# Kernel optimization log

Measured on AMD Instinct MI355X. Metric: run time of the kernel, lower is better.

Reference implementation:

```python
import jax, jax.numpy as jnp
import numpy as np

D_MODEL = 512
N_HEADS = 8
D_HEAD = D_MODEL // N_HEADS
N_LAYERS = 6
VOCAB = 32000
B, S = 4, 1024
EPS = 1e-5


def positional_encoding(length, d_model):
    # matches get_positional_encoding_table: pos * (1/10000**(i/d)), sin on even i, cos on odd i
    inv = 1.0 / (10000.0 ** (jnp.arange(d_model, dtype=jnp.float32) / d_model))
    ang = jnp.arange(length, dtype=jnp.float32)[:, None] * inv[None, :]  # [S, D]
    pe = jnp.where(jnp.arange(d_model) % 2 == 0, jnp.sin(ang), jnp.cos(ang))
    return pe


def layer_norm(x, g, b):
    m = jnp.mean(x, axis=-1, keepdims=True)
    v = jnp.mean((x - m) ** 2, axis=-1, keepdims=True)
    return (x - m) * jax.lax.rsqrt(v + EPS) * g + b


def setup_inputs() -> dict:
    key = jax.random.key(0)
    ks = jax.random.split(key, 9)
    sc = 0.02
    return {
        "tokens": jax.random.randint(ks[0], (B, S), 0, VOCAB),
        "emb": jax.random.normal(ks[1], (VOCAB, D_MODEL), jnp.float32) * sc,
        "Wq": jax.random.normal(ks[2], (N_LAYERS, D_MODEL, D_MODEL), jnp.float32) * sc,
        "bq": jnp.zeros((N_LAYERS, D_MODEL), jnp.float32),
        "Wk": jax.random.normal(ks[3], (N_LAYERS, D_MODEL, D_MODEL), jnp.float32) * sc,
        "bk": jnp.zeros((N_LAYERS, D_MODEL), jnp.float32),
        "Wv": jax.random.normal(ks[4], (N_LAYERS, D_MODEL, D_MODEL), jnp.float32) * sc,
        "bv": jnp.zeros((N_LAYERS, D_MODEL), jnp.float32),
        "Wo": jax.random.normal(ks[5], (N_LAYERS, D_MODEL, D_MODEL), jnp.float32) * sc,
        "bo": jnp.zeros((N_LAYERS, D_MODEL), jnp.float32),
        "W1": jax.random.normal(ks[6], (N_LAYERS, D_MODEL, 4 * D_MODEL), jnp.float32) * sc,
        "b1": jnp.zeros((N_LAYERS, 4 * D_MODEL), jnp.float32),
        "W2": jax.random.normal(ks[7], (N_LAYERS, 4 * D_MODEL, D_MODEL), jnp.float32) * sc,
        "b2": jnp.zeros((N_LAYERS, D_MODEL), jnp.float32),
        "ln_g": jnp.ones((N_LAYERS, D_MODEL), jnp.float32),
        "ln_b": jnp.zeros((N_LAYERS, D_MODEL), jnp.float32),
    }


def encoder_layer(x, Wq, bq, Wk, bk, Wv, bv, Wo, bo, W1, b1, W2, b2, g, b):
    bsz = x.shape[0]
    q = (x @ Wq + bq).reshape(bsz, -1, N_HEADS, D_HEAD).transpose(0, 2, 1, 3)  # [B,h,S,dk]
    k = (x @ Wk + bk).reshape(bsz, -1, N_HEADS, D_HEAD).transpose(0, 2, 1, 3)
    v = (x @ Wv + bv).reshape(bsz, -1, N_HEADS, D_HEAD).transpose(0, 2, 1, 3)
    scores = jnp.einsum('bhqd,bhkd->bhqk', q, k) / (D_HEAD ** 0.5)
    w = jax.nn.softmax(scores, axis=-1)
    attn = jnp.einsum('bhqk,bhkd->bhqd', w, v)  # [B,h,S,dv]
    # faithful to source bug: .view(B,-1,h*dv) WITHOUT transposing heads back
    attn = attn.reshape(bsz, -1, N_HEADS * D_HEAD)  # [B,S,D] with heads/seq interleaved
    x = layer_norm(x + (attn @ Wo + bo), g, b)
    ffn = jnp.maximum(x @ W1 + b1, 0.0) @ W2 + b2
    x = layer_norm(x + ffn, g, b)  # same (shared) LayerNorm params, as in source
    return x


def reference(tokens, emb, Wq, bq, Wk, bk, Wv, bv, Wo, bo, W1, b1, W2, b2, ln_g, ln_b):
    x = emb[tokens]  # [B,S,D]
    x = x + positional_encoding(x.shape[1], D_MODEL)
    for i in range(N_LAYERS):
        x = encoder_layer(x, Wq[i], bq[i], Wk[i], bk[i], Wv[i], bv[i], Wo[i], bo[i],
                          W1[i], b1[i], W2[i], b2[i], ln_g[i], ln_b[i])
    return x
```

## Files before the change

kernel.cpp:

```cpp
#include <hip/hip_runtime.h>
#include <hip/hip_bf16.h>
#include <math.h>

typedef unsigned short ushort_t;
typedef unsigned int uint_t;
typedef __attribute__((ext_vector_type(8))) short bfrag_t;
typedef __attribute__((ext_vector_type(4))) float facc_t;
typedef __attribute__((ext_vector_type(16))) float facc16_t;

#define D_MODEL 512
#define NH 8
#define DH 64
#define NL 6
#define BB 4
#define SS 1024
#define ROWS (BB*SS)
#define DFF 2048

__device__ inline ushort_t f2bf(float f) {
    __hip_bfloat16 h = __float2bfloat16(f);
    return *(ushort_t*)&h;
}
__device__ inline float bf2f(ushort_t u) {
    unsigned int x = ((unsigned int)u) << 16;
    union { unsigned int i; float f; } c; c.i = x;
    return c.f;
}
__device__ inline uint_t pkbf(float lo, float hi) {
    return (uint_t)f2bf(lo) | ((uint_t)f2bf(hi) << 16);
}
__device__ inline void gload_lds16(const void* g, void* l) {
    __builtin_amdgcn_global_load_lds((const __attribute__((address_space(1))) unsigned int*)g,
                                     (__attribute__((address_space(3))) unsigned int*)l, 16, 0, 0);
}

__global__ __launch_bounds__(256) void embed_pe(const int* __restrict__ tok,
                                                const float* __restrict__ emb,
                                                float* __restrict__ x,
                                                ushort_t* __restrict__ xbf) {
    int row = blockIdx.x;
    int s = row & (SS - 1);
    int t = tok[row];
    const float* e = emb + (size_t)t * D_MODEL;
    for (int i = threadIdx.x; i < D_MODEL; i += 256) {
        float freq = __expf(-9.210340371976184f * ((float)i / (float)D_MODEL));
        float ang = (float)s * freq;
        float pe = (i & 1) ? cosf(ang) : sinf(ang);
        float v = e[i] + pe;
        x[(size_t)row * D_MODEL + i] = v;
        xbf[(size_t)row * D_MODEL + i] = f2bf(v);
    }
}

__global__ __launch_bounds__(256) void prep_weights(const float* __restrict__ Wq,
                                                    const float* __restrict__ Wk,
                                                    const float* __restrict__ Wv,
                                                    const float* __restrict__ Wo,
                                                    const float* __restrict__ W1,
                                                    const float* __restrict__ W2,
                                                    int layer, ushort_t* __restrict__ wlay) {
    __shared__ float tile[32][33];
    int z = blockIdx.z;
    const float* src; ushort_t* dst; int K, N;
    size_t o512 = (size_t)layer * 512 * 512;
    size_t o1M  = (size_t)layer * 512 * 2048;
    switch (z) {
        case 0: src = Wq + o512; dst = wlay;               K = 512;  N = 512;  break;
        case 1: src = Wk + o512; dst = wlay + 262144;      K = 512;  N = 512;  break;
        case 2: src = Wv + o512; dst = wlay + 524288;      K = 512;  N = 512;  break;
        case 3: src = Wo + o512; dst = wlay + 786432;      K = 512;  N = 512;  break;
        case 4: src = W1 + o1M;  dst = wlay + 1048576;     K = 512;  N = 2048; break;
        default:src = W2 + o1M;  dst = wlay + 2097152;     K = 2048; N = 512;  break;
    }
    int n0 = blockIdx.x * 32, k0 = blockIdx.y * 32;
    if (n0 >= N || k0 >= K) return;
    int tx = threadIdx.x & 31, ty = threadIdx.x >> 5;
    #pragma unroll
    for (int i = 0; i < 4; i++)
        tile[ty + i * 8][tx] = src[(size_t)(k0 + ty + i * 8) * N + n0 + tx];
    __syncthreads();
    #pragma unroll
    for (int i = 0; i < 4; i++)
        dst[(size_t)(n0 + ty + i * 8) * K + k0 + tx] = f2bf(tile[tx][ty + i * 8]);
}

__global__ __launch_bounds__(256) void concat_bias(const float* __restrict__ bq,
                                                   const float* __restrict__ bk,
                                                   const float* __restrict__ bv,
                                                   float* __restrict__ bqkv) {
    int l = blockIdx.x;
    for (int i = threadIdx.x; i < 1536; i += 256) {
        float v = (i < 512) ? bq[l * 512 + i]
                : (i < 1024) ? bk[l * 512 + i - 512]
                : bv[l * 512 + i - 1024];
        bqkv[l * 1536 + i] = v;
    }
}

template<int BM, int BN>
__global__ __launch_bounds__(256) void gemm_pipe(const ushort_t* __restrict__ A,
                                                 const ushort_t* __restrict__ Bt,
                                                 const float* __restrict__ bias,
                                                 float* __restrict__ Cf,
                                                 ushort_t* __restrict__ Cb,
                                                 int N, int Ktot, int relu) {
    constexpr int TI = BM / 32, TJ = BN / 32;
    __shared__ ushort_t lA[2][BM * 64];
    __shared__ ushort_t lB[2][BN * 64];

    const int tid = threadIdx.x;
    const int w = tid >> 6, lane = tid & 63;
    const int wr = w & 1, wc = w >> 1;
    const int lane16 = lane & 15, quad = lane >> 4;
    const int row0 = blockIdx.y * BM, col0 = blockIdx.x * BN;

    facc_t acc[TI][TJ];
    #pragma unroll
    for (int i = 0; i < TI; i++)
        #pragma unroll
        for (int j = 0; j < TJ; j++)
            acc[i][j] = (facc_t){0.f, 0.f, 0.f, 0.f};

    auto stage = [&](int buf, int k0) {
        #pragma unroll
        for (int i = 0; i < BM / 32; i++) {
            int g = i * 256 + tid;
            int r = g >> 3, p = g & 7;
            int q = p ^ (r & 7);
            gload_lds16(A + (size_t)(row0 + r) * Ktot + k0 + q * 8,
                        lA[buf] + (size_t)g * 8);
        }
        #pragma unroll
        for (int i = 0; i < BN / 32; i++) {
            int g = i * 256 + tid;
            int r = g >> 3, p = g & 7;
            int q = p ^ (r & 7);
            gload_lds16(Bt + (size_t)(col0 + r) * Ktot + k0 + q * 8,
                        lB[buf] + (size_t)g * 8);
        }
    };
    auto compute = [&](int buf) {
        #pragma unroll
        for (int kk = 0; kk < 2; kk++) {
            bfrag_t af[TI], bf_[TJ];
            int q = kk * 4 + quad;
            #pragma unroll
            for (int t = 0; t < TI; t++) {
                int m = wr * (BM / 2) + t * 16 + lane16;
                af[t] = *(const bfrag_t*)(lA[buf] + ((size_t)m * 8 + (q ^ (m & 7))) * 8);
            }
            #pragma unroll
            for (int t = 0; t < TJ; t++) {
                int n = wc * (BN / 2) + t * 16 + lane16;
                bf_[t] = *(const bfrag_t*)(lB[buf] + ((size_t)n * 8 + (q ^ (n & 7))) * 8);
            }
            #pragma unroll
            for (int ti = 0; ti < TI; ti++)
                #pragma unroll
                for (int tj = 0; tj < TJ; tj++)
                    acc[ti][tj] = __builtin_amdgcn_mfma_f32_16x16x32_bf16(
                        af[ti], bf_[tj], acc[ti][tj], 0, 0, 0);
        }
    };

    const int nt = Ktot >> 6;
    stage(0, 0);
    __syncthreads();
    for (int t = 0; t < nt; t++) {
        if (t + 1 < nt) stage((t + 1) & 1, (t + 1) * 64);
        compute(t & 1);
        __syncthreads();
    }

    float bv_[TJ];
    #pragma unroll
    for (int tj = 0; tj < TJ; tj++)
        bv_[tj] = bias[col0 + wc * (BN / 2) + tj * 16 + lane16];

    #pragma unroll
    for (int ti = 0; ti < TI; ti++) {
        int grow = row0 + wr * (BM / 2) + ti * 16 + quad * 4;
        #pragma unroll
        for (int tj = 0; tj < TJ; tj++) {
            int gcol = col0 + wc * (BN / 2) + tj * 16 + lane16;
            #pragma unroll
            for (int rr = 0; rr < 4; rr++) {
                float v = acc[ti][tj][rr] + bv_[tj];
                if (relu) v = fmaxf(v, 0.f);
                size_t idx = (size_t)(grow + rr) * N + gcol;
                if (Cf) Cf[idx] = v;
                if (Cb) Cb[idx] = f2bf(v);
            }
        }
    }
}

__global__ __launch_bounds__(128) void attn_mfma_split(const ushort_t* __restrict__ qkv,
                                                       ushort_t* __restrict__ Yp,
                                                       float2* __restrict__ mlp) {
    __shared__ __align__(16) ushort_t lK[4096];
    __shared__ __align__(16) ushort_t lVT[2][4096];

    const int tid = threadIdx.x;
    const int w = tid >> 6, lane = tid & 63;
    const int l31 = lane & 31, H = lane >> 5;
    const int qt = blockIdx.x, h = blockIdx.y;
    const int b = blockIdx.z >> 1, kh = blockIdx.z & 1;
    const int kt0 = kh * 8;

    const float LOG2E = 1.4426950408889634f;
    const float SC = 0.125f * 1.4426950408889634f;

    const ushort_t* Qrow = qkv + (size_t)(b * SS + qt * 64 + w * 32 + l31) * 1536 + h * 64;
    bfrag_t qb[4];
    #pragma unroll
    for (int s = 0; s < 4; s++)
        qb[s] = *(const bfrag_t*)(Qrow + s * 16 + H * 8);

    facc16_t O0, O1;
    #pragma unroll
    for (int r = 0; r < 16; r++) { O0[r] = 0.f; O1[r] = 0.f; }
    float mrow = -INFINITY, lrow = 0.f;

    const int vkey = tid & 63;
    const int vdg  = tid >> 6;
    const int vk8 = vkey >> 3, vj = vkey & 7;

    auto stageK = [&](int kt) {
        #pragma unroll
        for (int i = 0; i < 4; i++) {
            int g = i * 128 + tid;
            int r = g >> 3, p = g & 7;
            int q = p ^ (r & 7);
            gload_lds16(qkv + (size_t)(b * SS + kt * 64 + r) * 1536 + h * 64 + 512 + q * 8,
                        lK + (size_t)g * 8);
        }
    };
    auto loadV = [&](int kt, ushort_t* vs) {
        const ushort_t* vsrc = qkv + (size_t)(b * SS + kt * 64 + vkey) * 1536
                               + h * 64 + 1024 + vdg * 32;
        #pragma unroll
        for (int i4 = 0; i4 < 4; i4++)
            *(uint4*)(vs + i4 * 8) = *(const uint4*)(vsrc + i4 * 8);
    };
    auto writeV = [&](const ushort_t* vs, int buf) {
        #pragma unroll
        for (int e = 0; e < 32; e++) {
            int n = vdg * 32 + e;
            lVT[buf][(size_t)(n * 8 + (vk8 ^ (n & 7))) * 8 + vj] = vs[e];
        }
    };

    {
        ushort_t v0[32];
        stageK(kt0);
        loadV(kt0, v0);
        writeV(v0, 0);
    }
    __syncthreads();

    for (int kt = kt0; kt < kt0 + 8; kt++) {
        const int buf = (kt - kt0) & 1;
        const bool more = (kt < kt0 + 7);

        ushort_t vn[32];
        if (more) loadV(kt + 1, vn);

        facc16_t sfv[2];
        #pragma unroll
        for (int half = 0; half < 2; half++) {
            facc16_t s_;
            #pragma unroll
            for (int r = 0; r < 16; r++) s_[r] = 0.f;
            int row = half * 32 + l31;
            #pragma unroll
            for (int s = 0; s < 4; s++) {
                int c = 2 * s + H;
                bfrag_t kf = *(const bfrag_t*)(lK + ((size_t)row * 8 + (c ^ (row & 7))) * 8);
                s_ = __builtin_amdgcn_mfma_f32_32x32x16_bf16(kf, qb[s], s_, 0, 0, 0);
            }
            sfv[half] = s_;
        }

        if (more) {
            __syncthreads();
            stageK(kt + 1);
        }

        #pragma unroll
        for (int half = 0; half < 2; half++) {
            facc16_t s_ = sfv[half];

            float mt = s_[0];
            #pragma unroll
            for (int r = 1; r < 16; r++) mt = fmaxf(mt, s_[r]);
            mt *= 0.125f;
            mt = fmaxf(mt, __shfl_xor(mt, 32));

            bool small = (mt <= mrow + 8.f);
            if (!__all(small)) {
                float mn = fmaxf(mrow, mt);
                float al = __builtin_amdgcn_exp2f((mrow - mn) * LOG2E);
                mrow = mn;
                lrow *= al;
                #pragma unroll
                for (int r = 0; r < 16; r++) { O0[r] *= al; O1[r] *= al; }
            }
            float mC = mrow * LOG2E;

            float p[16];
            float ps = 0.f;
            #pragma unroll
            for (int r = 0; r < 16; r++) {
                p[r] = __builtin_amdgcn_exp2f(fmaf(s_[r], SC, -mC));
                ps += p[r];
            }
            ps += __shfl_xor(ps, 32);
            lrow += ps;

            uint_t A0 = pkbf(p[0], p[1]),   A1 = pkbf(p[2], p[3]);
            uint_t B0 = pkbf(p[4], p[5]),   B1 = pkbf(p[6], p[7]);
            uint_t C0 = pkbf(p[8], p[9]),   C1 = pkbf(p[10], p[11]);
            uint_t D0 = pkbf(p[12], p[13]), D1 = pkbf(p[14], p[15]);
            uint_t XA0 = __shfl_xor(A0, 32), XA1 = __shfl_xor(A1, 32);
            uint_t XB0 = __shfl_xor(B0, 32), XB1 = __shfl_xor(B1, 32);
            uint_t XC0 = __shfl_xor(C0, 32), XC1 = __shfl_xor(C1, 32);
            uint_t XD0 = __shfl_xor(D0, 32), XD1 = __shfl_xor(D1, 32);

            union { bfrag_t v; uint_t u[4]; } pf0, pf1;
            pf0.u[0] = H ? XB0 : A0;  pf0.u[1] = H ? XB1 : A1;
            pf0.u[2] = H ? B0 : XA0;  pf0.u[3] = H ? B1 : XA1;
            pf1.u[0] = H ? XD0 : C0;  pf1.u[1] = H ? XD1 : C1;
            pf1.u[2] = H ? D0 : XC0;  pf1.u[3] = H ? D1 : XC1;

            #pragma unroll
            for (int t = 0; t < 2; t++) {
                int n = 32 * t + l31;
                #pragma unroll
                for (int ks = 0; ks < 2; ks++) {
                    int c = half * 4 + 2 * ks + H;
                    bfrag_t vf = *(const bfrag_t*)(&lVT[buf][((size_t)n * 8 + (c ^ (n & 7))) * 8]);
                    if (t == 0)
                        O0 = __builtin_amdgcn_mfma_f32_32x32x16_bf16(
                            vf, ks ? pf1.v : pf0.v, O0, 0, 0, 0);
                    else
                        O1 = __builtin_amdgcn_mfma_f32_32x32x16_bf16(
                            vf, ks ? pf1.v : pf0.v, O1, 0, 0, 0);
                }
            }
        }

        if (more) writeV(vn, buf ^ 1);

        __syncthreads();
    }

    size_t rbase = ((size_t)(kh * BB + b) * NH + h) * SS + qt * 64 + w * 32 + l31;
    float inv = 1.f / lrow;
    #pragma unroll
    for (int t = 0; t < 2; t++) {
        #pragma unroll
        for (int g = 0; g < 4; g++) {
            float v0 = (t ? O1[4 * g]     : O0[4 * g])     * inv;
            float v1 = (t ? O1[4 * g + 1] : O0[4 * g + 1]) * inv;
            float v2 = (t ? O1[4 * g + 2] : O0[4 * g + 2]) * inv;
            float v3 = (t ? O1[4 * g + 3] : O0[4 * g + 3]) * inv;
            uint2 pkd = make_uint2(pkbf(v0, v1), pkbf(v2, v3));
            *(uint2*)(Yp + rbase * DH + 32 * t + 8 * g + 4 * H) = pkd;
        }
    }
    if (H == 0)
        mlp[rbase] = make_float2(mrow, lrow);
}

__global__ __launch_bounds__(256) void attn_combine(const ushort_t* __restrict__ Yp,
                                                    const float2* __restrict__ mlp,
                                                    ushort_t* __restrict__ ab) {
    const float LOG2E = 1.4426950408889634f;
    int rid = blockIdx.x * 32 + (threadIdx.x >> 3);
    int d0 = (threadIdx.x & 7) * 8;
    float2 ml0 = mlp[rid];
    float2 ml1 = mlp[32768 + rid];
    float m = fmaxf(ml0.x, ml1.x);
    float a0 = __builtin_amdgcn_exp2f((ml0.x - m) * LOG2E) * ml0.y;
    float a1 = __builtin_amdgcn_exp2f((ml1.x - m) * LOG2E) * ml1.y;
    float inv = 1.f / (a0 + a1);
    a0 *= inv; a1 *= inv;
    uint4 u0 = *(const uint4*)(Yp + (size_t)rid * DH + d0);
    uint4 u1 = *(const uint4*)(Yp + (size_t)32768 * DH + (size_t)rid * DH + d0);
    const ushort_t* p0 = (const ushort_t*)&u0;
    const ushort_t* p1 = (const ushort_t*)&u1;
    ushort_t o[8];
    #pragma unroll
    for (int e = 0; e < 8; e++)
        o[e] = f2bf(a0 * bf2f(p0[e]) + a1 * bf2f(p1[e]));
    *(uint4*)(ab + (size_t)rid * DH + d0) = *(uint4*)o;
}

__global__ __launch_bounds__(256) void add_ln(const float* __restrict__ x,
                                              const float* __restrict__ delta,
                                              const float* __restrict__ g,
                                              const float* __restrict__ bparm,
                                              float* __restrict__ outf,
                                              ushort_t* __restrict__ outb) {
    __shared__ float red[2][4];
    int row = blockIdx.x;
    int t = threadIdx.x;
    const float* xr = x + (size_t)row * D_MODEL;
    const float* dr = delta + (size_t)row * D_MODEL;
    float v0 = xr[t] + dr[t];
    float v1 = xr[t + 256] + dr[t + 256];
    float s = v0 + v1;
    float ss = v0 * v0 + v1 * v1;
    #pragma unroll
    for (int off = 1; off < 64; off <<= 1) {
        s  += __shfl_xor(s, off);
        ss += __shfl_xor(ss, off);
    }
    int lane = t & 63, wid = t >> 6;
    if (lane == 0) { red[0][wid] = s; red[1][wid] = ss; }
    __syncthreads();
    s  = red[0][0] + red[0][1] + red[0][2] + red[0][3];
    ss = red[1][0] + red[1][1] + red[1][2] + red[1][3];
    float mean = s * (1.f / D_MODEL);
    float var = ss * (1.f / D_MODEL) - mean * mean;
    float rinv = rsqrtf(var + 1e-5f);
    float o0 = (v0 - mean) * rinv * g[t]       + bparm[t];
    float o1 = (v1 - mean) * rinv * g[t + 256] + bparm[t + 256];
    float* orow = outf + (size_t)row * D_MODEL;
    orow[t] = o0; orow[t + 256] = o1;
    ushort_t* brow = outb + (size_t)row * D_MODEL;
    brow[t] = f2bf(o0); brow[t + 256] = f2bf(o1);
}

extern "C" void kernel_launch(void* const* d_in, const int* in_sizes, int n_in,
                              void* d_out, int out_size, void* d_ws, size_t ws_size,
                              hipStream_t stream) {
    const int* tokens = (const int*)d_in[0];
    const float* emb = (const float*)d_in[1];
    const float* Wq = (const float*)d_in[2];  const float* bq = (const float*)d_in[3];
    const float* Wk = (const float*)d_in[4];  const float* bk = (const float*)d_in[5];
    const float* Wv = (const float*)d_in[6];  const float* bv = (const float*)d_in[7];
    const float* Wo = (const float*)d_in[8];  const float* bo = (const float*)d_in[9];
    const float* W1 = (const float*)d_in[10]; const float* b1 = (const float*)d_in[11];
    const float* W2 = (const float*)d_in[12]; const float* b2 = (const float*)d_in[13];
    const float* lng = (const float*)d_in[14]; const float* lnb = (const float*)d_in[15];

    char* base = (char*)d_ws;
    ushort_t* wlay = (ushort_t*)(base);
    float*    bqkv = (float*)   (base + 6291456);
    float*    x    = (float*)   (base + 6328320);
    ushort_t* xbf  = (ushort_t*)(base + 14716928);
    float*    tmp  = (float*)   (base + 18911232);
    ushort_t* qkv  = (ushort_t*)(base + 27299840);
    ushort_t* ab   = (ushort_t*)(base + 39882752);
    ushort_t* mid  = qkv;

    ushort_t* Yp  = (ushort_t*)tmp;
    float2*   mlp = (float2*)xbf;

    ushort_t* wqkv_t = wlay;
    ushort_t* wo_t   = wlay + 786432;
    ushort_t* w1_t   = wlay + 1048576;
    ushort_t* w2_t   = wlay + 2097152;

    concat_bias<<<NL, 256, 0, stream>>>(bq, bk, bv, bqkv);
    embed_pe<<<ROWS, 256, 0, stream>>>(tokens, emb, x, xbf);

    for (int l = 0; l < NL; l++) {
        prep_weights<<<dim3(64, 64, 6), 256, 0, stream>>>(Wq, Wk, Wv, Wo, W1, W2, l, wlay);

        gemm_pipe<128, 128><<<dim3(12, 32), 256, 0, stream>>>(
            xbf, wqkv_t, bqkv + l * 1536, nullptr, qkv, 1536, 512, 0);

        attn_mfma_split<<<dim3(16, NH, BB * 2), 128, 0, stream>>>(qkv, Yp, mlp);
        attn_combine<<<1024, 256, 0, stream>>>(Yp, mlp, ab);

        gemm_pipe<64, 64><<<dim3(8, 64), 256, 0, stream>>>(
            ab, wo_t, bo + l * D_MODEL, tmp, nullptr, 512, 512, 0);
        add_ln<<<ROWS, 256, 0, stream>>>(x, tmp, lng + l * D_MODEL, lnb + l * D_MODEL,
                                         x, xbf);

        gemm_pipe<128, 128><<<dim3(16, 32), 256, 0, stream>>>(
            xbf, w1_t, b1 + l * DFF, nullptr, mid, 2048, 512, 1);

        gemm_pipe<64, 64><<<dim3(8, 64), 256, 0, stream>>>(
            mid, w2_t, b2 + l * D_MODEL, tmp, nullptr, 512, 2048, 0);

        float* lnout = (l == NL - 1) ? (float*)d_out : x;
        add_ln<<<ROWS, 256, 0, stream>>>(x, tmp, lng + l * D_MODEL, lnb + l * D_MODEL,
                                         lnout, xbf);
    }
}
```

Measured before the change: 881.9 us.

## Split-K the FFN down-projection and pass bf16 residual deltas to LayerNorm

Adds a split-K template parameter to the GEMM and runs the W2 GEMM (K=2048) as two K halves that write separate bf16 partial outputs. The add+LayerNorm kernel now reads and sums these bf16 partials in place of one fp32 delta. The Wo GEMM output also becomes bf16, and the QKV GEMM switches to 128x64 tiles for more blocks. This aims to raise parallelism on the long-K GEMM and halve delta traffic, at the cost of rounding the residual deltas to bf16.

New measurement: 856.5 us. 2.9% less time.

```diff
diff --git a/kernel.cpp b/kernel.cpp
--- a/kernel.cpp
+++ b/kernel.cpp
@@ -97,12 +97,13 @@
     }
 }
 
-template<int BM, int BN>
+template<int BM, int BN, int SPLIT>
 __global__ __launch_bounds__(256) void gemm_pipe(const ushort_t* __restrict__ A,
                                                  const ushort_t* __restrict__ Bt,
                                                  const float* __restrict__ bias,
                                                  float* __restrict__ Cf,
-                                                 ushort_t* __restrict__ Cb,
+                                                 ushort_t* __restrict__ Cb0,
+                                                 ushort_t* __restrict__ Cb1,
                                                  int N, int Ktot, int relu) {
     constexpr int TI = BM / 32, TJ = BN / 32;
     __shared__ ushort_t lA[2][BM * 64];
@@ -113,6 +114,9 @@
     const int wr = w & 1, wc = w >> 1;
     const int lane16 = lane & 15, quad = lane >> 4;
     const int row0 = blockIdx.y * BM, col0 = blockIdx.x * BN;
+    const int kz = (SPLIT > 1) ? blockIdx.z : 0;
+    const int Ks = Ktot / SPLIT;
+    const int kbeg = kz * Ks;
 
     facc_t acc[TI][TJ];
     #pragma unroll
@@ -127,7 +131,7 @@
             int g = i * 256 + tid;
             int r = g >> 3, p = g & 7;
             int q = p ^ (r & 7);
-            gload_lds16(A + (size_t)(row0 + r) * Ktot + k0 + q * 8,
+            gload_lds16(A + (size_t)(row0 + r) * Ktot + kbeg + k0 + q * 8,
                         lA[buf] + (size_t)g * 8);
         }
         #pragma unroll
@@ -135,7 +139,7 @@
             int g = i * 256 + tid;
             int r = g >> 3, p = g & 7;
             int q = p ^ (r & 7);
-            gload_lds16(Bt + (size_t)(col0 + r) * Ktot + k0 + q * 8,
+            gload_lds16(Bt + (size_t)(col0 + r) * Ktot + kbeg + k0 + q * 8,
                         lB[buf] + (size_t)g * 8);
         }
     };
@@ -163,7 +167,7 @@
         }
     };
 
-    const int nt = Ktot >> 6;
+    const int nt = Ks >> 6;
     stage(0, 0);
     __syncthreads();
     for (int t = 0; t < nt; t++) {
@@ -175,7 +179,10 @@
     float bv_[TJ];
     #pragma unroll
     for (int tj = 0; tj < TJ; tj++)
-        bv_[tj] = bias[col0 + wc * (BN / 2) + tj * 16 + lane16];
+        bv_[tj] = (SPLIT > 1 && kz != 0) ? 0.f
+                 : bias[col0 + wc * (BN / 2) + tj * 16 + lane16];
+
+    ushort_t* Cb = (SPLIT > 1 && kz != 0) ? Cb1 : Cb0;
 
     #pragma unroll
     for (int ti = 0; ti < TI; ti++) {
@@ -397,19 +404,28 @@
     *(uint4*)(ab + (size_t)rid * DH + d0) = *(uint4*)o;
 }
 
-__global__ __launch_bounds__(256) void add_ln(const float* __restrict__ x,
-                                              const float* __restrict__ delta,
-                                              const float* __restrict__ g,
-                                              const float* __restrict__ bparm,
-                                              float* __restrict__ outf,
-                                              ushort_t* __restrict__ outb) {
+template<int NP>
+__global__ __launch_bounds__(256) void add_lnb(const float* __restrict__ x,
+                                               const ushort_t* __restrict__ d0,
+                                               const ushort_t* __restrict__ d1,
+                                               const float* __restrict__ g,
+                                               const float* __restrict__ bparm,
+                                               float* __restrict__ outf,
+                                               ushort_t* __restrict__ outb) {
     __shared__ float red[2][4];
     int row = blockIdx.x;
     int t = threadIdx.x;
     const float* xr = x + (size_t)row * D_MODEL;
-    const float* dr = delta + (size_t)row * D_MODEL;
-    float v0 = xr[t] + dr[t];
-    float v1 = xr[t + 256] + dr[t + 256];
+    const ushort_t* dr0 = d0 + (size_t)row * D_MODEL;
+    float del0 = bf2f(dr0[t]);
+    float del1 = bf2f(dr0[t + 256]);
+    if (NP == 2) {
+        const ushort_t* dr1 = d1 + (size_t)row * D_MODEL;
+        del0 += bf2f(dr1[t]);
+        del1 += bf2f(dr1[t + 256]);
+    }
+    float v0 = xr[t] + del0;
+    float v1 = xr[t + 256] + del1;
     float s = v0 + v1;
     float ss = v0 * v0 + v1 * v1;
     #pragma unroll
@@ -456,8 +472,10 @@
     ushort_t* ab   = (ushort_t*)(base + 39882752);
     ushort_t* mid  = qkv;
 
-    ushort_t* Yp  = (ushort_t*)tmp;
-    float2*   mlp = (float2*)xbf;
+    ushort_t* Yp   = (ushort_t*)tmp;
+    float2*   mlp  = (float2*)xbf;
+    ushort_t* dlt0 = (ushort_t*)tmp;
+    ushort_t* dlt1 = (ushort_t*)tmp + 2097152;
 
     ushort_t* wqkv_t = wlay;
     ushort_t* wo_t   = wlay + 786432;
@@ -470,25 +488,27 @@
     for (int l = 0; l < NL; l++) {
         prep_weights<<<dim3(64, 64, 6), 256, 0, stream>>>(Wq, Wk, Wv, Wo, W1, W2, l, wlay);
 
-        gemm_pipe<128, 128><<<dim3(12, 32), 256, 0, stream>>>(
-            xbf, wqkv_t, bqkv + l * 1536, nullptr, qkv, 1536, 512, 0);
+        gemm_pipe<128, 64, 1><<<dim3(24, 32), 256, 0, stream>>>(
+            xbf, wqkv_t, bqkv + l * 1536, nullptr, qkv, nullptr, 1536, 512, 0);
 
         attn_mfma_split<<<dim3(16, NH, BB * 2), 128, 0, stream>>>(qkv, Yp, mlp);
         attn_combine<<<1024, 256, 0, stream>>>(Yp, mlp, ab);
 
-        gemm_pipe<64, 64><<<dim3(8, 64), 256, 0, stream>>>(
-            ab, wo_t, bo + l * D_MODEL, tmp, nullptr, 512, 512, 0);
-        add_ln<<<ROWS, 256, 0, stream>>>(x, tmp, lng + l * D_MODEL, lnb + l * D_MODEL,
-                                         x, xbf);
-
-        gemm_pipe<128, 128><<<dim3(16, 32), 256, 0, stream>>>(
-            xbf, w1_t, b1 + l * DFF, nullptr, mid, 2048, 512, 1);
-
-        gemm_pipe<64, 64><<<dim3(8, 64), 256, 0, stream>>>(
-            mid, w2_t, b2 + l * D_MODEL, tmp, nullptr, 512, 2048, 0);
+        gemm_pipe<64, 64, 1><<<dim3(8, 64), 256, 0, stream>>>(
+            ab, wo_t, bo + l * D_MODEL, nullptr, dlt0, nullptr, 512, 512, 0);
+        add_lnb<1><<<ROWS, 256, 0, stream>>>(x, dlt0, nullptr,
+                                             lng + l * D_MODEL, lnb + l * D_MODEL,
+                                             x, xbf);
+
+        gemm_pipe<128, 128, 1><<<dim3(16, 32), 256, 0, stream>>>(
+            xbf, w1_t, b1 + l * DFF, nullptr, mid, nullptr, 2048, 512, 1);
+
+        gemm_pipe<64, 64, 2><<<dim3(8, 64, 2), 256, 0, stream>>>(
+            mid, w2_t, b2 + l * D_MODEL, nullptr, dlt0, dlt1, 512, 2048, 0);
 
         float* lnout = (l == NL - 1) ? (float*)d_out : x;
-        add_ln<<<ROWS, 256, 0, stream>>>(x, tmp, lng + l * D_MODEL, lnb + l * D_MODEL,
-                                         lnout, xbf);
-    }
-}
+        add_lnb<2><<<ROWS, 256, 0, stream>>>(x, dlt0, dlt1,
+                                             lng + l * D_MODEL, lnb + l * D_MODEL,
+                                             lnout, xbf);
+    }
+}
```
